# Kernel tuning notes

Hardware: AMD Instinct MI355X
Metric: run time of the kernel (lower is better)

The kernel has to match this reference:

```python
import jax, jax.numpy as jnp
import numpy as np

N = 100000   # num nodes
E = 1200000  # num edges
D = 64       # embedding dim
K = 3        # propagation hops (alpha has K+1 entries)


def setup_inputs() -> dict:
    key = jax.random.key(0)
    k1, k2, k3 = jax.random.split(key, 3)
    edge_index = jax.random.randint(k1, (2, E), 0, N, dtype=jnp.int64)
    weight = jax.random.normal(k2, (N, D), dtype=jnp.float32)
    alpha = jax.random.uniform(k3, (K + 1,), dtype=jnp.float32)
    return {"edge_index": edge_index, "weight": weight, "alpha": alpha}


def reference(edge_index, weight, alpha):
    row = edge_index[0]  # source j
    col = edge_index[1]  # target i
    # symmetric normalization: in-degree over col, deg^-1/2 with inf -> 0
    deg = jax.ops.segment_sum(jnp.ones((E,), dtype=weight.dtype), col, num_segments=N)
    dinv = jnp.where(deg == 0, 0.0, deg ** -0.5)
    edge_w = dinv[row] * dinv[col]  # [E]

    out = weight * alpha[0]
    x = weight
    for k in range(1, K + 1):
        # gather-scale-scatter propagation hop
        msg = edge_w[:, None] * x[row]                      # [E, D]
        x = jax.ops.segment_sum(msg, col, num_segments=N)   # [N, D]
        out = out + x * alpha[k]

    # per-edge link scores: dot(out[src], out[dst])
    return jnp.sum(out[row] * out[col], axis=-1)  # [E]
```

## Files before the change

### kernel.cpp

```cpp
#include <hip/hip_runtime.h>
#include <hip/hip_bf16.h>

#define GN 100000
#define GE 1200000
#define GD 64
#define NG 256
#define CPG 391
#define CAP 6144


__global__ void detect_kernel(const void* __restrict__ w,
                              const void* __restrict__ edge,
                              int* __restrict__ flags, int* __restrict__ gcount) {
    __shared__ int s_badw, s_edgenz;
    if (threadIdx.x == 0) { s_badw = 0; s_edgenz = 0; }
    gcount[threadIdx.x] = 0;
    __syncthreads();
    const unsigned short* wh = (const unsigned short*)w;
    const unsigned int*   ei = (const unsigned int*)edge;
    int badw = 0, edgenz = 0;
    for (int i = threadIdx.x; i < 4096; i += 256) {
        unsigned int bits = ((unsigned int)wh[i]) << 16;
        float v = __uint_as_float(bits);
        if (!(fabsf(v) <= 100.0f)) badw = 1;
        if ((i & 1) == 1 && ei[i] != 0u) edgenz = 1;
    }
    if (badw)   atomicOr(&s_badw, 1);
    if (edgenz) atomicOr(&s_edgenz, 1);
    __syncthreads();
    if (threadIdx.x == 0) {
        flags[0] = s_badw ? 0 : 1;
        flags[1] = s_edgenz ? 0 : 1;
    }
}

__device__ __forceinline__ int ld_row(const int* __restrict__ edge, int e, int e64) {
    return e64 ? edge[2 * (size_t)e] : edge[e];
}
__device__ __forceinline__ int ld_col(const int* __restrict__ edge, int e, int e64) {
    return e64 ? edge[2 * ((size_t)GE + (size_t)e)] : edge[(size_t)GE + (size_t)e];
}
__device__ __forceinline__ float ld_f(const void* __restrict__ p, size_t i, int bf16f) {
    if (bf16f) return __bfloat162float(((const __hip_bfloat16*)p)[i]);
    return ((const float*)p)[i];
}

__device__ __forceinline__ float bf_lo(unsigned u) { return __uint_as_float(u << 16); }
__device__ __forceinline__ float bf_hi(unsigned u) { return __uint_as_float(u & 0xFFFF0000u); }
__device__ __forceinline__ unsigned bf16bits(float f) {
    __hip_bfloat16 h = __float2bfloat16(f);
    unsigned short s;
    __builtin_memcpy(&s, &h, 2);
    return (unsigned)s;
}

__global__ void p1_kernel(const int* __restrict__ edge, const int* __restrict__ flags,
                          int* __restrict__ gcount, unsigned* __restrict__ bucket,
                          int E, int chunk) {
    __shared__ int cnt[NG];
    __shared__ int base[NG];
    int t = threadIdx.x;
    int e64 = flags[1];
    cnt[t] = 0;
    __syncthreads();
    int lo = blockIdx.x * chunk;
    int hiE = min(lo + chunk, E);
    for (int e = lo + t; e < hiE; e += 256) {
        int c = ld_col(edge, e, e64);
        int r = ld_row(edge, e, e64);
        if ((unsigned)c < (unsigned)GN && (unsigned)r < (unsigned)GN)
            atomicAdd(&cnt[c / CPG], 1);
    }
    __syncthreads();
    int cv = cnt[t];
    base[t] = (cv > 0) ? atomicAdd(&gcount[t], cv) : 0;
    __syncthreads();
    cnt[t] = 0;
    __syncthreads();
    for (int e = lo + t; e < hiE; e += 256) {
        int c = ld_col(edge, e, e64);
        int r = ld_row(edge, e, e64);
        if ((unsigned)c < (unsigned)GN && (unsigned)r < (unsigned)GN) {
            int g = c / CPG;
            int idx = base[g] + atomicAdd(&cnt[g], 1);
            if (idx < CAP)
                bucket[(size_t)g * CAP + idx] = ((unsigned)(c - g * CPG) << 17) | (unsigned)r;
        }
    }
}

__global__ void p2_kernel(const unsigned* __restrict__ bucket, const int* __restrict__ gcount,
                          int* __restrict__ rowptr, float* __restrict__ dinv,
                          int* __restrict__ csr) {
    int g = blockIdx.x;
    int t = threadIdx.x;
    __shared__ int gs[NG];
    __shared__ int hist[512];
    __shared__ int s[512];
    int gv = gcount[t]; if (gv > CAP) gv = CAP;
    gs[t] = gv;
    hist[t] = 0; hist[t + 256] = 0;
    __syncthreads();
    for (int off = 1; off < NG; off <<= 1) {
        int u = (t >= off) ? gs[t - off] : 0;
        __syncthreads();
        gs[t] += u;
        __syncthreads();
    }
    int mg = gcount[g]; if (mg > CAP) mg = CAP;
    int gb = gs[g] - mg;
    int m = mg;
    const unsigned* bk = bucket + (size_t)g * CAP;
    for (int idx = t; idx < m; idx += 256)
        atomicAdd(&hist[bk[idx] >> 17], 1);
    __syncthreads();
    int h0 = hist[t], h1 = hist[t + 256];
    s[t] = h0; s[t + 256] = h1;
    __syncthreads();
    for (int off = 1; off < 512; off <<= 1) {
        int v0 = (t >= off) ? s[t - off] : 0;
        int v1 = (t + 256 >= off) ? s[t + 256 - off] : 0;
        __syncthreads();
        s[t] += v0; s[t + 256] += v1;
        __syncthreads();
    }
    int col0 = g * CPG + t;
    int col1 = col0 + 256;
    if (col0 < GN) {
        rowptr[col0] = gb + s[t];
        dinv[col0] = (h0 > 0) ? rsqrtf((float)h0) : 0.0f;
    }
    if (t + 256 < CPG && col1 < GN) {
        rowptr[col1] = gb + s[t + 256];
        dinv[col1] = (h1 > 0) ? rsqrtf((float)h1) : 0.0f;
    }
    __syncthreads();
    hist[t] = s[t] - h0;
    hist[t + 256] = s[t + 256] - h1;
    __syncthreads();
    for (int idx = t; idx < m; idx += 256) {
        unsigned u = bk[idx];
        int cl = u >> 17;
        int r  = (int)(u & 0x1FFFFu);
        int pos = gb + atomicAdd(&hist[cl], 1);
        csr[pos] = r;
    }
}

__global__ void init_kernel(const void* __restrict__ w, const void* __restrict__ alpha,
                            const int* __restrict__ flags,
                            __hip_bfloat16* __restrict__ X, __hip_bfloat16* __restrict__ OUT,
                            int n) {
    int i = 4 * (blockIdx.x * blockDim.x + threadIdx.x);
    int wbf = flags[0];
    if (i < n) {
        float a0 = ld_f(alpha, 0, wbf);
        #pragma unroll
        for (int q = 0; q < 4; ++q) {
            float v = ld_f(w, i + q, wbf);
            X[i + q] = __float2bfloat16(v);
            OUT[i + q] = __float2bfloat16(a0 * v);
        }
    }
}

__global__ void gather_kernel(const __hip_bfloat16* __restrict__ X,
                              __hip_bfloat16* __restrict__ Y,
                              __hip_bfloat16* __restrict__ OUT,
                              const int* __restrict__ rowptr, const int* __restrict__ csr,
                              const float* __restrict__ dinv,
                              const void* __restrict__ alpha, const int* __restrict__ flags,
                              int k, int store_y, int N) {
    int t = blockIdx.x * blockDim.x + threadIdx.x;
    int node = __builtin_amdgcn_readfirstlane(t >> 6);
    if (node >= N) return;
    int lane = t & 63;
    int h = lane >> 4;
    int i = lane & 15;
    int beg = node ? rowptr[node - 1] : 0;
    int end = rowptr[node];
    float dc = dinv[node];
    float a = ld_f(alpha, k, flags[0]);
    size_t obase = (size_t)node * GD + 4 * i;
    uint2 uo = *(const uint2*)(OUT + obase);
    float f0 = 0.0f, f1 = 0.0f, f2 = 0.0f, f3 = 0.0f;
    for (int j = beg; j < end; j += 16) {
        int i0 = j + 0 + h;  int i1 = j + 4 + h;
        int i2 = j + 8 + h;  int i3 = j + 12 + h;
        int last = end - 1;
        int r0 = csr[min(i0, last)];
        int r1 = csr[min(i1, last)];
        int r2 = csr[min(i2, last)];
        int r3 = csr[min(i3, last)];
        float w0 = (i0 < end) ? dinv[r0] : 0.0f;
        float w1 = (i1 < end) ? dinv[r1] : 0.0f;
        float w2 = (i2 < end) ? dinv[r2] : 0.0f;
        float w3 = (i3 < end) ? dinv[r3] : 0.0f;
        uint2 u0 = *(const uint2*)(X + (size_t)r0 * GD + 4 * i);
        uint2 u1 = *(const uint2*)(X + (size_t)r1 * GD + 4 * i);
        uint2 u2 = *(const uint2*)(X + (size_t)r2 * GD + 4 * i);
        uint2 u3 = *(const uint2*)(X + (size_t)r3 * GD + 4 * i);
        f0 = fmaf(w0, bf_lo(u0.x), f0); f1 = fmaf(w0, bf_hi(u0.x), f1);
        f2 = fmaf(w0, bf_lo(u0.y), f2); f3 = fmaf(w0, bf_hi(u0.y), f3);
        f0 = fmaf(w1, bf_lo(u1.x), f0); f1 = fmaf(w1, bf_hi(u1.x), f1);
        f2 = fmaf(w1, bf_lo(u1.y), f2); f3 = fmaf(w1, bf_hi(u1.y), f3);
        f0 = fmaf(w2, bf_lo(u2.x), f0); f1 = fmaf(w2, bf_hi(u2.x), f1);
        f2 = fmaf(w2, bf_lo(u2.y), f2); f3 = fmaf(w2, bf_hi(u2.y), f3);
        f0 = fmaf(w3, bf_lo(u3.x), f0); f1 = fmaf(w3, bf_hi(u3.x), f1);
        f2 = fmaf(w3, bf_lo(u3.y), f2); f3 = fmaf(w3, bf_hi(u3.y), f3);
    }
    f0 += __shfl_xor(f0, 16, 64); f0 += __shfl_xor(f0, 32, 64);
    f1 += __shfl_xor(f1, 16, 64); f1 += __shfl_xor(f1, 32, 64);
    f2 += __shfl_xor(f2, 16, 64); f2 += __shfl_xor(f2, 32, 64);
    f3 += __shfl_xor(f3, 16, 64); f3 += __shfl_xor(f3, 32, 64);
    f0 *= dc; f1 *= dc; f2 *= dc; f3 *= dc;
    if (h == 0) {
        if (store_y) {
            uint2 p;
            p.x = (bf16bits(f1) << 16) | bf16bits(f0);
            p.y = (bf16bits(f3) << 16) | bf16bits(f2);
            *(uint2*)(Y + obase) = p;
        }
        float o0 = fmaf(a, f0, bf_lo(uo.x));
        float o1 = fmaf(a, f1, bf_hi(uo.x));
        float o2 = fmaf(a, f2, bf_lo(uo.y));
        float o3 = fmaf(a, f3, bf_hi(uo.y));
        uint2 q;
        q.x = (bf16bits(o1) << 16) | bf16bits(o0);
        q.y = (bf16bits(o3) << 16) | bf16bits(o2);
        *(uint2*)(OUT + obase) = q;
    }
}

__device__ __forceinline__ float dot2_bf16(unsigned ua, unsigned ub) {
    return fmaf(bf_lo(ua), bf_lo(ub), bf_hi(ua) * bf_hi(ub));
}

__global__ void dot_kernel(const __hip_bfloat16* __restrict__ OUT,
                           const int* __restrict__ edge, const int* __restrict__ flags,
                           void* __restrict__ res, int E) {
    int t = blockIdx.x * blockDim.x + threadIdx.x;
    int e = t >> 2;
    int sub = t & 3;
    if (e >= E) return;
    int e64 = flags[1];
    int wbf = flags[0];
    int r = ld_row(edge, e, e64);
    int c = ld_col(edge, e, e64);
    float p = 0.0f;
    if ((unsigned)r < (unsigned)GN && (unsigned)c < (unsigned)GN) {
        const uint4* pa = (const uint4*)(OUT + (size_t)r * GD + sub * 16);
        const uint4* pb = (const uint4*)(OUT + (size_t)c * GD + sub * 16);
        uint4 a0 = pa[0], a1 = pa[1];
        uint4 b0 = pb[0], b1 = pb[1];
        p = ((dot2_bf16(a0.x, b0.x) + dot2_bf16(a0.y, b0.y)) +
             (dot2_bf16(a0.z, b0.z) + dot2_bf16(a0.w, b0.w))) +
            ((dot2_bf16(a1.x, b1.x) + dot2_bf16(a1.y, b1.y)) +
             (dot2_bf16(a1.z, b1.z) + dot2_bf16(a1.w, b1.w)));
    }
    p += __shfl_down(p, 2, 4);
    p += __shfl_down(p, 1, 4);
    if (sub == 0) {
        if (wbf) ((__hip_bfloat16*)res)[e] = __float2bfloat16(p);
        else     ((float*)res)[e] = p;
    }
}

extern "C" void kernel_launch(void* const* d_in, const int* in_sizes, int n_in,
                              void* d_out, int out_size, void* d_ws, size_t ws_size,
                              hipStream_t stream) {
    const int E = GE, N = GN, ND = GN * GD;

    const void* edge   = d_in[0];
    const void* weight = d_in[1];
    const void* alpha  = d_in[2];

    char* ws = (char*)d_ws;
    int*      flags     = (int*)ws;      ws += 256;
    int*      gcount    = (int*)ws;      ws += 1024;
    float*    dinv      = (float*)ws;    ws += (((size_t)N * 4 + 255) / 256) * 256;
    int*      rowptr    = (int*)ws;      ws += (((size_t)N * 4 + 255) / 256) * 256;
    unsigned* bucket    = (unsigned*)ws; ws += (size_t)NG * CAP * 4;
    int*      csr       = (int*)ws;      ws += (size_t)E * 4;
    __hip_bfloat16* X   = (__hip_bfloat16*)ws; ws += (size_t)ND * 2;
    __hip_bfloat16* Y   = (__hip_bfloat16*)ws; ws += (size_t)ND * 2;
    __hip_bfloat16* OUT = (__hip_bfloat16*)ws; ws += (size_t)ND * 2;

    const int B = 256;

    detect_kernel<<<1, 256, 0, stream>>>(weight, edge, flags, gcount);

    {
        const int P1B = 256;
        const int chunk = (E + P1B - 1) / P1B;
        p1_kernel<<<P1B, 256, 0, stream>>>((const int*)edge, flags, gcount, bucket, E, chunk);
    }
    p2_kernel<<<NG, 256, 0, stream>>>(bucket, gcount, rowptr, dinv, csr);

    init_kernel<<<(ND / 4 + B - 1) / B, B, 0, stream>>>(weight, alpha, flags, X, OUT, ND);

    const int ggrid = (int)(((size_t)N * 64 + B - 1) / B);
    gather_kernel<<<ggrid, B, 0, stream>>>(X, Y, OUT, rowptr, csr, dinv, alpha, flags, 1, 1, N);
    gather_kernel<<<ggrid, B, 0, stream>>>(Y, X, OUT, rowptr, csr, dinv, alpha, flags, 2, 1, N);
    gather_kernel<<<ggrid, B, 0, stream>>>(X, Y, OUT, rowptr, csr, dinv, alpha, flags, 3, 0, N);

    dot_kernel<<<(int)(((size_t)E * 4 + B - 1) / B), B, 0, stream>>>(OUT, (const int*)edge, flags, d_out, E);
}
```

Measured before the change: 286.9 us.

## Fuse init into bucketing kernel and gather first hop from raw weights

The separate init kernel is folded into the edge-bucketing kernel as extra blocks, which saves a launch and lets the init work overlap with bucketing. The init no longer writes a bf16 copy of the weights. The first propagation hop instead reads the original fp32 weights directly, converting on load when the input is not bf16. This cuts one full N×D write, but the first hop now gathers twice the bytes per row from fp32 rows.

```diff
diff --git a/kernel.cpp b/kernel.cpp
--- a/kernel.cpp
+++ b/kernel.cpp
@@ -54,37 +54,56 @@
     return (unsigned)s;
 }
 
-__global__ void p1_kernel(const int* __restrict__ edge, const int* __restrict__ flags,
-                          int* __restrict__ gcount, unsigned* __restrict__ bucket,
-                          int E, int chunk) {
-    __shared__ int cnt[NG];
-    __shared__ int base[NG];
-    int t = threadIdx.x;
-    int e64 = flags[1];
-    cnt[t] = 0;
-    __syncthreads();
-    int lo = blockIdx.x * chunk;
-    int hiE = min(lo + chunk, E);
-    for (int e = lo + t; e < hiE; e += 256) {
-        int c = ld_col(edge, e, e64);
-        int r = ld_row(edge, e, e64);
-        if ((unsigned)c < (unsigned)GN && (unsigned)r < (unsigned)GN)
-            atomicAdd(&cnt[c / CPG], 1);
-    }
-    __syncthreads();
-    int cv = cnt[t];
-    base[t] = (cv > 0) ? atomicAdd(&gcount[t], cv) : 0;
-    __syncthreads();
-    cnt[t] = 0;
-    __syncthreads();
-    for (int e = lo + t; e < hiE; e += 256) {
-        int c = ld_col(edge, e, e64);
-        int r = ld_row(edge, e, e64);
-        if ((unsigned)c < (unsigned)GN && (unsigned)r < (unsigned)GN) {
-            int g = c / CPG;
-            int idx = base[g] + atomicAdd(&cnt[g], 1);
-            if (idx < CAP)
-                bucket[(size_t)g * CAP + idx] = ((unsigned)(c - g * CPG) << 17) | (unsigned)r;
+__global__ void p1init_kernel(const int* __restrict__ edge, const int* __restrict__ flags,
+                              int* __restrict__ gcount, unsigned* __restrict__ bucket,
+                              int E, int chunk,
+                              const void* __restrict__ w, const void* __restrict__ alpha,
+                              __hip_bfloat16* __restrict__ OUT, int nd) {
+    if (blockIdx.x < NG) {
+        __shared__ int cnt[NG];
+        __shared__ int base[NG];
+        int t = threadIdx.x;
+        int e64 = flags[1];
+        cnt[t] = 0;
+        __syncthreads();
+        int lo = blockIdx.x * chunk;
+        int hiE = min(lo + chunk, E);
+        for (int e = lo + t; e < hiE; e += 256) {
+            int c = ld_col(edge, e, e64);
+            int r = ld_row(edge, e, e64);
+            if ((unsigned)c < (unsigned)GN && (unsigned)r < (unsigned)GN)
+                atomicAdd(&cnt[c / CPG], 1);
+        }
+        __syncthreads();
+        int cv = cnt[t];
+        base[t] = (cv > 0) ? atomicAdd(&gcount[t], cv) : 0;
+        __syncthreads();
+        cnt[t] = 0;
+        __syncthreads();
+        for (int e = lo + t; e < hiE; e += 256) {
+            int c = ld_col(edge, e, e64);
+            int r = ld_row(edge, e, e64);
+            if ((unsigned)c < (unsigned)GN && (unsigned)r < (unsigned)GN) {
+                int g = c / CPG;
+                int idx = base[g] + atomicAdd(&cnt[g], 1);
+                if (idx < CAP)
+                    bucket[(size_t)g * CAP + idx] = ((unsigned)(c - g * CPG) << 17) | (unsigned)r;
+            }
+        }
+    } else {
+        int bid = blockIdx.x - NG;
+        int i = 4 * (bid * 256 + (int)threadIdx.x);
+        int wbf = flags[0];
+        if (i < nd) {
+            float a0 = ld_f(alpha, 0, wbf);
+            float v0 = ld_f(w, i + 0, wbf);
+            float v1 = ld_f(w, i + 1, wbf);
+            float v2 = ld_f(w, i + 2, wbf);
+            float v3 = ld_f(w, i + 3, wbf);
+            uint2 q;
+            q.x = (bf16bits(a0 * v1) << 16) | bf16bits(a0 * v0);
+            q.y = (bf16bits(a0 * v3) << 16) | bf16bits(a0 * v2);
+            *(uint2*)(OUT + i) = q;
         }
     }
 }
@@ -147,36 +166,32 @@
     }
 }
 
-__global__ void init_kernel(const void* __restrict__ w, const void* __restrict__ alpha,
-                            const int* __restrict__ flags,
-                            __hip_bfloat16* __restrict__ X, __hip_bfloat16* __restrict__ OUT,
-                            int n) {
-    int i = 4 * (blockIdx.x * blockDim.x + threadIdx.x);
-    int wbf = flags[0];
-    if (i < n) {
-        float a0 = ld_f(alpha, 0, wbf);
-        #pragma unroll
-        for (int q = 0; q < 4; ++q) {
-            float v = ld_f(w, i + q, wbf);
-            X[i + q] = __float2bfloat16(v);
-            OUT[i + q] = __float2bfloat16(a0 * v);
-        }
-    }
-}
-
-__global__ void gather_kernel(const __hip_bfloat16* __restrict__ X,
+__device__ __forceinline__ float4 ld_xrow(const void* __restrict__ Xp, int r, int i, int asf32) {
+    float4 o;
+    if (asf32) {
+        const float* p = (const float*)Xp + (size_t)r * GD + 4 * i;
+        o.x = p[0]; o.y = p[1]; o.z = p[2]; o.w = p[3];
+    } else {
+        uint2 u = *(const uint2*)((const __hip_bfloat16*)Xp + (size_t)r * GD + 4 * i);
+        o.x = bf_lo(u.x); o.y = bf_hi(u.x); o.z = bf_lo(u.y); o.w = bf_hi(u.y);
+    }
+    return o;
+}
+
+__global__ void gather_kernel(const void* __restrict__ Xsrc,
                               __hip_bfloat16* __restrict__ Y,
                               __hip_bfloat16* __restrict__ OUT,
                               const int* __restrict__ rowptr, const int* __restrict__ csr,
                               const float* __restrict__ dinv,
                               const void* __restrict__ alpha, const int* __restrict__ flags,
-                              int k, int store_y, int N) {
+                              int k, int store_y, int src_is_w, int N) {
     int t = blockIdx.x * blockDim.x + threadIdx.x;
     int node = __builtin_amdgcn_readfirstlane(t >> 6);
     if (node >= N) return;
     int lane = t & 63;
     int h = lane >> 4;
     int i = lane & 15;
+    int asf32 = src_is_w && !flags[0];
     int beg = node ? rowptr[node - 1] : 0;
     int end = rowptr[node];
     float dc = dinv[node];
@@ -196,18 +211,18 @@
         float w1 = (i1 < end) ? dinv[r1] : 0.0f;
         float w2 = (i2 < end) ? dinv[r2] : 0.0f;
         float w3 = (i3 < end) ? dinv[r3] : 0.0f;
-        uint2 u0 = *(const uint2*)(X + (size_t)r0 * GD + 4 * i);
-        uint2 u1 = *(const uint2*)(X + (size_t)r1 * GD + 4 * i);
-        uint2 u2 = *(const uint2*)(X + (size_t)r2 * GD + 4 * i);
-        uint2 u3 = *(const uint2*)(X + (size_t)r3 * GD + 4 * i);
-        f0 = fmaf(w0, bf_lo(u0.x), f0); f1 = fmaf(w0, bf_hi(u0.x), f1);
-        f2 = fmaf(w0, bf_lo(u0.y), f2); f3 = fmaf(w0, bf_hi(u0.y), f3);
-        f0 = fmaf(w1, bf_lo(u1.x), f0); f1 = fmaf(w1, bf_hi(u1.x), f1);
-        f2 = fmaf(w1, bf_lo(u1.y), f2); f3 = fmaf(w1, bf_hi(u1.y), f3);
-        f0 = fmaf(w2, bf_lo(u2.x), f0); f1 = fmaf(w2, bf_hi(u2.x), f1);
-        f2 = fmaf(w2, bf_lo(u2.y), f2); f3 = fmaf(w2, bf_hi(u2.y), f3);
-        f0 = fmaf(w3, bf_lo(u3.x), f0); f1 = fmaf(w3, bf_hi(u3.x), f1);
-        f2 = fmaf(w3, bf_lo(u3.y), f2); f3 = fmaf(w3, bf_hi(u3.y), f3);
+        float4 x0 = ld_xrow(Xsrc, r0, i, asf32);
+        float4 x1 = ld_xrow(Xsrc, r1, i, asf32);
+        float4 x2 = ld_xrow(Xsrc, r2, i, asf32);
+        float4 x3 = ld_xrow(Xsrc, r3, i, asf32);
+        f0 = fmaf(w0, x0.x, f0); f1 = fmaf(w0, x0.y, f1);
+        f2 = fmaf(w0, x0.z, f2); f3 = fmaf(w0, x0.w, f3);
+        f0 = fmaf(w1, x1.x, f0); f1 = fmaf(w1, x1.y, f1);
+        f2 = fmaf(w1, x1.z, f2); f3 = fmaf(w1, x1.w, f3);
+        f0 = fmaf(w2, x2.x, f0); f1 = fmaf(w2, x2.y, f1);
+        f2 = fmaf(w2, x2.z, f2); f3 = fmaf(w2, x2.w, f3);
+        f0 = fmaf(w3, x3.x, f0); f1 = fmaf(w3, x3.y, f1);
+        f2 = fmaf(w3, x3.z, f2); f3 = fmaf(w3, x3.w, f3);
     }
     f0 += __shfl_xor(f0, 16, 64); f0 += __shfl_xor(f0, 32, 64);
     f1 += __shfl_xor(f1, 16, 64); f1 += __shfl_xor(f1, 32, 64);
@@ -282,8 +297,8 @@
     int*      rowptr    = (int*)ws;      ws += (((size_t)N * 4 + 255) / 256) * 256;
     unsigned* bucket    = (unsigned*)ws; ws += (size_t)NG * CAP * 4;
     int*      csr       = (int*)ws;      ws += (size_t)E * 4;
-    __hip_bfloat16* X   = (__hip_bfloat16*)ws; ws += (size_t)ND * 2;
     __hip_bfloat16* Y   = (__hip_bfloat16*)ws; ws += (size_t)ND * 2;
+    __hip_bfloat16* X2  = (__hip_bfloat16*)ws; ws += (size_t)ND * 2;
     __hip_bfloat16* OUT = (__hip_bfloat16*)ws; ws += (size_t)ND * 2;
 
     const int B = 256;
@@ -291,18 +306,18 @@
     detect_kernel<<<1, 256, 0, stream>>>(weight, edge, flags, gcount);
 
     {
-        const int P1B = 256;
-        const int chunk = (E + P1B - 1) / P1B;
-        p1_kernel<<<P1B, 256, 0, stream>>>((const int*)edge, flags, gcount, bucket, E, chunk);
+        const int chunk = (E + NG - 1) / NG;
+        const int initBlocks = (ND / 4 + B - 1) / B;
+        p1init_kernel<<<NG + initBlocks, B, 0, stream>>>(
+            (const int*)edge, flags, gcount, bucket, E, chunk,
+            weight, alpha, OUT, ND);
     }
     p2_kernel<<<NG, 256, 0, stream>>>(bucket, gcount, rowptr, dinv, csr);
 
-    init_kernel<<<(ND / 4 + B - 1) / B, B, 0, stream>>>(weight, alpha, flags, X, OUT, ND);
-
     const int ggrid = (int)(((size_t)N * 64 + B - 1) / B);
-    gather_kernel<<<ggrid, B, 0, stream>>>(X, Y, OUT, rowptr, csr, dinv, alpha, flags, 1, 1, N);
-    gather_kernel<<<ggrid, B, 0, stream>>>(Y, X, OUT, rowptr, csr, dinv, alpha, flags, 2, 1, N);
-    gather_kernel<<<ggrid, B, 0, stream>>>(X, Y, OUT, rowptr, csr, dinv, alpha, flags, 3, 0, N);
+    gather_kernel<<<ggrid, B, 0, stream>>>(weight, Y, OUT, rowptr, csr, dinv, alpha, flags, 1, 1, 1, N);
+    gather_kernel<<<ggrid, B, 0, stream>>>(Y, X2, OUT, rowptr, csr, dinv, alpha, flags, 2, 1, 0, N);
+    gather_kernel<<<ggrid, B, 0, stream>>>(X2, Y, OUT, rowptr, csr, dinv, alpha, flags, 3, 0, 0, N);
 
     dot_kernel<<<(int)(((size_t)E * 4 + B - 1) / B), B, 0, stream>>>(OUT, (const int*)edge, flags, d_out, E);
 }
```

New measurement: 319.7 us. 1.11x slower.
